# Performance work log

Measured on AMD Instinct MI355X. Metric: run time of the kernel, lower is better.

Reference implementation:

```python
import jax, jax.numpy as jnp
import numpy as np

B, D, H, E = 32768, 128, 512, 16

def setup_inputs() -> dict:
    key = jax.random.key(0)
    ks = jax.random.split(key, 5)
    x = jax.random.normal(ks[0], (B, 1, D), dtype=jnp.float32)
    s1 = 1.0 / float(np.sqrt(H))   # init_ uses last-dim size: w1 last dim = H
    s2 = 1.0 / float(np.sqrt(D))   # w2 last dim = D
    sg = 1.0 / float(np.sqrt(D))   # nn.Linear(D, E) default init scale
    w1 = jax.random.uniform(ks[1], (E, D, H), minval=-s1, maxval=s1, dtype=jnp.float32)
    w2 = jax.random.uniform(ks[2], (E, H, D), minval=-s2, maxval=s2, dtype=jnp.float32)
    wg = jax.random.uniform(ks[3], (D, E), minval=-sg, maxval=sg, dtype=jnp.float32)
    bg = jax.random.uniform(ks[4], (E,), minval=-sg, maxval=sg, dtype=jnp.float32)
    return {"x": x, "w1": w1, "w2": w2, "wg": wg, "bg": bg}

def reference(x, w1, w2, wg, bg):
    xt = x[:, 0, :]                                   # (B, D); seq dim is 1 by construction
    logits = xt @ wg + bg                             # (B, E)
    topk_vals, topk_idx = jax.lax.top_k(logits, 1)    # (B, 1) each
    scores = jax.nn.softmax(topk_vals, axis=-1)       # (B, 1); all ones for k=1
    # every expert processes every token (faithful to the reference)
    hidden = jax.nn.gelu(jnp.einsum('bd,edh->ebh', xt, w1), approximate=False)  # (E, B, H)
    eout = jnp.einsum('ebh,ehd->ebd', hidden, w2)     # (E, B, D)
    # gather selected expert per token, scale, sum over k
    sel = jnp.take_along_axis(eout.transpose(1, 0, 2), topk_idx[:, :, None], axis=1)  # (B, 1, D)
    return (sel * scores[:, :, None]).sum(axis=1)     # (B, D)
```

## Files before the change

kernel.cpp:

```cpp
#include <hip/hip_runtime.h>
#include <hip/hip_bf16.h>
#include <math.h>

#define NB 32768
#define DD 128
#define HH 512
#define EE 16
#define TM 64
#define HC 32
#define NCH (HH / HC)

typedef __attribute__((ext_vector_type(8))) short short8;
typedef __attribute__((ext_vector_type(4))) float f32x4;

__device__ __forceinline__ unsigned short f2bf(float f) {
  union { float f; unsigned u; } v; v.f = f;
  unsigned r = v.u + 0x7fffu + ((v.u >> 16) & 1u);
  return (unsigned short)(r >> 16);
}

__device__ __forceinline__ float fast_erf(float z) {
  float a = fabsf(z);
  float t = 1.0f / (1.0f + 0.3275911f * a);
  float y = t * (0.254829592f + t * (-0.284496736f + t * (1.421413741f +
            t * (-1.453152027f + t * 1.061405429f))));
  float r = 1.0f - y * __expf(-a * a);
  return z < 0.0f ? -r : r;
}

__global__ __launch_bounds__(256) void prep_kernel(
    const float* __restrict__ x, const float* __restrict__ wg,
    const float* __restrict__ bg, const float* __restrict__ w1,
    const float* __restrict__ w2, int* __restrict__ counts,
    int* __restrict__ rows, unsigned short* __restrict__ w1T,
    unsigned short* __restrict__ w2T) {
  __shared__ __align__(16) char smem[50816];
  int tid = threadIdx.x;

  if (blockIdx.x >= 512) {
    float (*tile)[65] = (float (*)[65])smem;
    int tp = blockIdx.x - 512;
    const float* src; unsigned short* dst; int S, Sd;
    if (tp < 256) {
      int e = tp >> 4, t2 = tp & 15;
      int d0 = (t2 >> 3) * 64, h0 = (t2 & 7) * 64;
      src = w1 + (size_t)e * DD * HH + (size_t)d0 * HH + h0; S = HH;
      dst = w1T + (size_t)e * HH * DD + (size_t)h0 * DD + d0; Sd = DD;
    } else {
      int t = tp - 256;
      int e = t >> 4, t2 = t & 15;
      int h0 = (t2 >> 1) * 64, d0 = (t2 & 1) * 64;
      src = w2 + (size_t)e * HH * DD + (size_t)h0 * DD + d0; S = DD;
      dst = w2T + (size_t)e * DD * HH + (size_t)d0 * HH + h0; Sd = HH;
    }
    #pragma unroll
    for (int i = 0; i < 4; ++i) {
      int u = tid + i * 256, r = u >> 4, c = (u & 15) * 4;
      float4 v = *(const float4*)(src + (size_t)r * S + c);
      tile[r][c + 0] = v.x; tile[r][c + 1] = v.y;
      tile[r][c + 2] = v.z; tile[r][c + 3] = v.w;
    }
    __syncthreads();
    #pragma unroll
    for (int i = 0; i < 4; ++i) {
      int u = tid + i * 256, tr = u >> 4, tc = (u & 15) * 4;
      ushort4 p;
      p.x = f2bf(tile[tc + 0][tr]); p.y = f2bf(tile[tc + 1][tr]);
      p.z = f2bf(tile[tc + 2][tr]); p.w = f2bf(tile[tc + 3][tr]);
      *(ushort4*)(dst + (size_t)tr * Sd + tc) = p;
    }
    return;
  }

  float  (*sx)[132] = (float (*)[132])smem;
  double (*swg)[EE] = (double (*)[EE])(smem + 33792);
  int* lcnt  = (int*)(smem + 50176);
  int* gbase = lcnt + EE;
  int* lslot = gbase + EE;
  int* lexp  = lslot + 64;

  int base = blockIdx.x * 64;
  if (tid < EE) lcnt[tid] = 0;
  for (int i = tid; i < DD * EE; i += 256) swg[i >> 4][i & 15] = (double)wg[i];
  {
    int r = tid >> 2, c0 = (tid & 3) * 32;
    const float4* src = (const float4*)(x + (size_t)(base + r) * DD + c0);
    #pragma unroll
    for (int i = 0; i < 8; ++i)
      *(float4*)&sx[r][c0 + i * 4] = src[i];
  }
  __syncthreads();

  int r = tid >> 2;
  int e0 = (tid & 3) * 4;
  double acc[4];
  #pragma unroll
  for (int j = 0; j < 4; ++j) acc[j] = (double)bg[e0 + j];

  #pragma unroll 4
  for (int d = 0; d < DD; ++d) {
    double xv = (double)sx[r][d];
    #pragma unroll
    for (int j = 0; j < 4; ++j)
      acc[j] += xv * swg[d][e0 + j];
  }

  int beste = 0; double bestv = acc[0];
  #pragma unroll
  for (int j = 1; j < 4; ++j)
    if (acc[j] > bestv) { bestv = acc[j]; beste = j; }
  int ge = e0 + beste;

  #pragma unroll
  for (int off = 1; off < 4; off <<= 1) {
    double ov = __shfl_xor(bestv, off);
    int oe = __shfl_xor(ge, off);
    if (ov > bestv || (ov == bestv && oe < ge)) { bestv = ov; ge = oe; }
  }

  if ((tid & 3) == 0) {
    lslot[r] = atomicAdd(&lcnt[ge], 1);
    lexp[r] = ge;
  }
  __syncthreads();
  if (tid < EE && lcnt[tid] > 0)
    gbase[tid] = atomicAdd(&counts[tid], lcnt[tid]);
  __syncthreads();
  if ((tid & 3) == 0) {
    int e2 = lexp[r];
    rows[e2 * NB + gbase[e2] + lslot[r]] = base + r;
  }
}

__global__ __launch_bounds__(256) void moe_gemm(
    const float* __restrict__ x, const unsigned short* __restrict__ w1T,
    const unsigned short* __restrict__ w2T, const int* __restrict__ counts,
    const int* __restrict__ rows, float* __restrict__ out) {
  int e = blockIdx.x;
  int cnt = counts[e];
  int base = blockIdx.y * TM;
  if (base >= cnt) return;

  __shared__ unsigned short sW1[2][HC][DD];
  __shared__ unsigned short sW2[2][DD][HC];
  __shared__ unsigned short sH[TM][HC];

  int tid = threadIdx.x;
  int wv = tid >> 6, l = tid & 63;
  int lm = l & 15, q = l >> 4;

  short8 xa[4];
  {
    int ridx = base + wv * 16 + lm; if (ridx >= cnt) ridx = cnt - 1;
    int grow = rows[e * NB + ridx];
    const float* xr = x + (size_t)grow * DD + q * 8;
    #pragma unroll
    for (int ks = 0; ks < 4; ++ks) {
      f32x4 v0 = *(const f32x4*)(xr + ks * 32);
      f32x4 v1 = *(const f32x4*)(xr + ks * 32 + 4);
      short8 a;
      a[0] = f2bf(v0[0]); a[1] = f2bf(v0[1]); a[2] = f2bf(v0[2]); a[3] = f2bf(v0[3]);
      a[4] = f2bf(v1[0]); a[5] = f2bf(v1[1]); a[6] = f2bf(v1[2]); a[7] = f2bf(v1[3]);
      xa[ks] = a;
    }
  }

  int r1s = tid >> 4, s1s = tid & 15;
  int sl1 = (s1s ^ (r1s & 7)) * 8;
  int r2s = tid >> 2, s2s = tid & 3;
  int sl2 = (s2s ^ ((r2s >> 1) & 3)) * 8;

  {
    const unsigned short* w1c = w1T + (size_t)e * HH * DD;
    const unsigned short* w2c = w2T + (size_t)e * DD * HH;
    uint4 a0 = *(const uint4*)(w1c + (size_t)tid * 8);
    uint4 a1 = *(const uint4*)(w1c + (size_t)(tid + 256) * 8);
    uint4 b0 = *(const uint4*)(w2c + (size_t)r2s * HH + s2s * 8);
    uint4 b1 = *(const uint4*)(w2c + (size_t)(r2s + 64) * HH + s2s * 8);
    *(uint4*)&sW1[0][r1s][sl1]      = a0;
    *(uint4*)&sW1[0][r1s + 16][sl1] = a1;
    *(uint4*)&sW2[0][r2s][sl2]      = b0;
    *(uint4*)&sW2[0][r2s + 64][sl2] = b1;
  }
  __syncthreads();

  f32x4 acc2[8];
  #pragma unroll
  for (int n = 0; n < 8; ++n) acc2[n] = (f32x4){0.f, 0.f, 0.f, 0.f};

  for (int hc = 0; hc < NCH; ++hc) {
    int b = hc & 1;

    uint4 pa0, pa1, pb0, pb1;
    if (hc + 1 < NCH) {
      const unsigned short* w1c = w1T + ((size_t)e * HH + (size_t)(hc + 1) * HC) * DD;
      const unsigned short* w2c = w2T + (size_t)e * DD * HH + (size_t)(hc + 1) * HC;
      pa0 = *(const uint4*)(w1c + (size_t)tid * 8);
      pa1 = *(const uint4*)(w1c + (size_t)(tid + 256) * 8);
      pb0 = *(const uint4*)(w2c + (size_t)r2s * HH + s2s * 8);
      pb1 = *(const uint4*)(w2c + (size_t)(r2s + 64) * HH + s2s * 8);
    }

    f32x4 acc1[2];
    #pragma unroll
    for (int n = 0; n < 2; ++n) acc1[n] = (f32x4){0.f, 0.f, 0.f, 0.f};
    #pragma unroll
    for (int ks = 0; ks < 4; ++ks) {
      #pragma unroll
      for (int n = 0; n < 2; ++n) {
        int row = n * 16 + lm;
        int sl = ((ks * 4 + q) ^ (row & 7)) * 8;
        short8 bfr = *(const short8*)&sW1[b][row][sl];
        acc1[n] = __builtin_amdgcn_mfma_f32_16x16x32_bf16(xa[ks], bfr, acc1[n], 0, 0, 0);
      }
    }
    #pragma unroll
    for (int n = 0; n < 2; ++n) {
      #pragma unroll
      for (int rr = 0; rr < 4; ++rr) {
        float v = acc1[n][rr];
        float g = 0.5f * v * (1.0f + fast_erf(v * 0.70710678118654752f));
        int row = wv * 16 + q * 4 + rr;
        int col = n * 16 + lm;
        int sl = ((col >> 3) ^ ((row >> 1) & 3)) * 8;
        sH[row][sl + (col & 7)] = f2bf(g);
      }
    }
    {
      int rowA = wv * 16 + lm;
      int slA = (q ^ ((rowA >> 1) & 3)) * 8;
      short8 a = *(const short8*)&sH[rowA][slA];
      #pragma unroll
      for (int n = 0; n < 8; ++n) {
        int row = n * 16 + lm;
        int sl = (q ^ ((row >> 1) & 3)) * 8;
        short8 bfr = *(const short8*)&sW2[b][row][sl];
        acc2[n] = __builtin_amdgcn_mfma_f32_16x16x32_bf16(a, bfr, acc2[n], 0, 0, 0);
      }
    }

    if (hc + 1 < NCH) {
      *(uint4*)&sW1[b ^ 1][r1s][sl1]      = pa0;
      *(uint4*)&sW1[b ^ 1][r1s + 16][sl1] = pa1;
      *(uint4*)&sW2[b ^ 1][r2s][sl2]      = pb0;
      *(uint4*)&sW2[b ^ 1][r2s + 64][sl2] = pb1;
    }
    __syncthreads();
  }

  #pragma unroll
  for (int rr = 0; rr < 4; ++rr) {
    int ml = wv * 16 + q * 4 + rr;
    int ridx = base + ml;
    if (ridx < cnt) {
      int grow = rows[e * NB + ridx];
      float* op = out + (size_t)grow * DD + lm;
      #pragma unroll
      for (int n = 0; n < 8; ++n) op[n * 16] = acc2[n][rr];
    }
  }
}

extern "C" void kernel_launch(void* const* d_in, const int* in_sizes, int n_in,
                              void* d_out, int out_size, void* d_ws, size_t ws_size,
                              hipStream_t stream) {
  const float* x  = (const float*)d_in[0];
  const float* w1 = (const float*)d_in[1];
  const float* w2 = (const float*)d_in[2];
  const float* wg = (const float*)d_in[3];
  const float* bg = (const float*)d_in[4];
  float* out = (float*)d_out;

  int* counts = (int*)d_ws;
  int* rows   = (int*)((char*)d_ws + 1024);
  unsigned short* w1T = (unsigned short*)((char*)d_ws + 1024 + (size_t)EE * NB * 4);
  unsigned short* w2T = w1T + (size_t)EE * HH * DD;

  hipMemsetAsync(d_ws, 0, 64, stream);
  hipLaunchKernelGGL(prep_kernel, dim3(1024), dim3(256), 0, stream,
                     x, wg, bg, w1, w2, counts, rows, w1T, w2T);
  hipLaunchKernelGGL(moe_gemm, dim3(EE, NB / TM), dim3(256), 0, stream,
                     x, w1T, w2T, counts, rows, out);
}
```

Before: 135.6 us.

## Double hidden chunk size to 64, re-swizzle LDS tiles, and use fast reciprocal in erf

Measured after the change: 170.8 us. +26.0%, slower.

```diff
diff --git a/kernel.cpp b/kernel.cpp
--- a/kernel.cpp
+++ b/kernel.cpp
@@ -7,7 +7,7 @@
 #define HH 512
 #define EE 16
 #define TM 64
-#define HC 32
+#define HC 64
 #define NCH (HH / HC)
 
 typedef __attribute__((ext_vector_type(8))) short short8;
@@ -21,7 +21,7 @@
 
 __device__ __forceinline__ float fast_erf(float z) {
   float a = fabsf(z);
-  float t = 1.0f / (1.0f + 0.3275911f * a);
+  float t = __builtin_amdgcn_rcpf(1.0f + 0.3275911f * a);
   float y = t * (0.254829592f + t * (-0.284496736f + t * (1.421413741f +
             t * (-1.453152027f + t * 1.061405429f))));
   float r = 1.0f - y * __expf(-a * a);
@@ -132,7 +132,7 @@
   }
 }
 
-__global__ __launch_bounds__(256) void moe_gemm(
+__global__ __launch_bounds__(256, 2) void moe_gemm(
     const float* __restrict__ x, const unsigned short* __restrict__ w1T,
     const unsigned short* __restrict__ w2T, const int* __restrict__ counts,
     const int* __restrict__ rows, float* __restrict__ out) {
@@ -143,7 +143,7 @@
 
   __shared__ unsigned short sW1[2][HC][DD];
   __shared__ unsigned short sW2[2][DD][HC];
-  __shared__ unsigned short sH[TM][HC];
+  __shared__ unsigned short sH[TM][72];
 
   int tid = threadIdx.x;
   int wv = tid >> 6, l = tid & 63;
@@ -168,19 +168,26 @@
   int r1s = tid >> 4, s1s = tid & 15;
   int sl1 = (s1s ^ (r1s & 7)) * 8;
   int r2s = tid >> 2, s2s = tid & 3;
-  int sl2 = (s2s ^ ((r2s >> 1) & 3)) * 8;
+  int sl2a = ((2 * s2s)     ^ (r2s & 7)) * 8;
+  int sl2b = ((2 * s2s + 1) ^ (r2s & 7)) * 8;
+
+  const unsigned short* w1e = w1T + (size_t)e * HH * DD;
+  const unsigned short* w2e = w2T + (size_t)e * DD * HH;
 
   {
-    const unsigned short* w1c = w1T + (size_t)e * HH * DD;
-    const unsigned short* w2c = w2T + (size_t)e * DD * HH;
-    uint4 a0 = *(const uint4*)(w1c + (size_t)tid * 8);
-    uint4 a1 = *(const uint4*)(w1c + (size_t)(tid + 256) * 8);
-    uint4 b0 = *(const uint4*)(w2c + (size_t)r2s * HH + s2s * 8);
-    uint4 b1 = *(const uint4*)(w2c + (size_t)(r2s + 64) * HH + s2s * 8);
-    *(uint4*)&sW1[0][r1s][sl1]      = a0;
-    *(uint4*)&sW1[0][r1s + 16][sl1] = a1;
-    *(uint4*)&sW2[0][r2s][sl2]      = b0;
-    *(uint4*)&sW2[0][r2s + 64][sl2] = b1;
+    #pragma unroll
+    for (int k = 0; k < 4; ++k) {
+      uint4 a = *(const uint4*)(w1e + (size_t)tid * 8 + (size_t)k * 2048);
+      *(uint4*)&sW1[0][r1s + 16 * k][sl1] = a;
+    }
+    uint4 b0 = *(const uint4*)(w2e + (size_t)r2s * HH + s2s * 16);
+    uint4 b1 = *(const uint4*)(w2e + (size_t)r2s * HH + s2s * 16 + 8);
+    uint4 b2 = *(const uint4*)(w2e + (size_t)(r2s + 64) * HH + s2s * 16);
+    uint4 b3 = *(const uint4*)(w2e + (size_t)(r2s + 64) * HH + s2s * 16 + 8);
+    *(uint4*)&sW2[0][r2s][sl2a]      = b0;
+    *(uint4*)&sW2[0][r2s][sl2b]      = b1;
+    *(uint4*)&sW2[0][r2s + 64][sl2a] = b2;
+    *(uint4*)&sW2[0][r2s + 64][sl2b] = b3;
   }
   __syncthreads();
 
@@ -191,23 +198,26 @@
   for (int hc = 0; hc < NCH; ++hc) {
     int b = hc & 1;
 
-    uint4 pa0, pa1, pb0, pb1;
+    uint4 pa[4], pb[4];
     if (hc + 1 < NCH) {
-      const unsigned short* w1c = w1T + ((size_t)e * HH + (size_t)(hc + 1) * HC) * DD;
-      const unsigned short* w2c = w2T + (size_t)e * DD * HH + (size_t)(hc + 1) * HC;
-      pa0 = *(const uint4*)(w1c + (size_t)tid * 8);
-      pa1 = *(const uint4*)(w1c + (size_t)(tid + 256) * 8);
-      pb0 = *(const uint4*)(w2c + (size_t)r2s * HH + s2s * 8);
-      pb1 = *(const uint4*)(w2c + (size_t)(r2s + 64) * HH + s2s * 8);
-    }
-
-    f32x4 acc1[2];
-    #pragma unroll
-    for (int n = 0; n < 2; ++n) acc1[n] = (f32x4){0.f, 0.f, 0.f, 0.f};
+      const unsigned short* w1c = w1e + (size_t)(hc + 1) * HC * DD;
+      const unsigned short* w2c = w2e + (size_t)(hc + 1) * HC;
+      #pragma unroll
+      for (int k = 0; k < 4; ++k)
+        pa[k] = *(const uint4*)(w1c + (size_t)tid * 8 + (size_t)k * 2048);
+      pb[0] = *(const uint4*)(w2c + (size_t)r2s * HH + s2s * 16);
+      pb[1] = *(const uint4*)(w2c + (size_t)r2s * HH + s2s * 16 + 8);
+      pb[2] = *(const uint4*)(w2c + (size_t)(r2s + 64) * HH + s2s * 16);
+      pb[3] = *(const uint4*)(w2c + (size_t)(r2s + 64) * HH + s2s * 16 + 8);
+    }
+
+    f32x4 acc1[4];
+    #pragma unroll
+    for (int n = 0; n < 4; ++n) acc1[n] = (f32x4){0.f, 0.f, 0.f, 0.f};
     #pragma unroll
     for (int ks = 0; ks < 4; ++ks) {
       #pragma unroll
-      for (int n = 0; n < 2; ++n) {
+      for (int n = 0; n < 4; ++n) {
         int row = n * 16 + lm;
         int sl = ((ks * 4 + q) ^ (row & 7)) * 8;
         short8 bfr = *(const short8*)&sW1[b][row][sl];
@@ -215,35 +225,35 @@
       }
     }
     #pragma unroll
-    for (int n = 0; n < 2; ++n) {
+    for (int n = 0; n < 4; ++n) {
       #pragma unroll
       for (int rr = 0; rr < 4; ++rr) {
         float v = acc1[n][rr];
         float g = 0.5f * v * (1.0f + fast_erf(v * 0.70710678118654752f));
-        int row = wv * 16 + q * 4 + rr;
-        int col = n * 16 + lm;
-        int sl = ((col >> 3) ^ ((row >> 1) & 3)) * 8;
-        sH[row][sl + (col & 7)] = f2bf(g);
+        sH[wv * 16 + q * 4 + rr][n * 16 + lm] = f2bf(g);
       }
     }
-    {
-      int rowA = wv * 16 + lm;
-      int slA = (q ^ ((rowA >> 1) & 3)) * 8;
-      short8 a = *(const short8*)&sH[rowA][slA];
+    #pragma unroll
+    for (int ks = 0; ks < 2; ++ks) {
+      int kk = ks * 32 + q * 8;
+      short8 a = *(const short8*)&sH[wv * 16 + lm][kk];
       #pragma unroll
       for (int n = 0; n < 8; ++n) {
         int row = n * 16 + lm;
-        int sl = (q ^ ((row >> 1) & 3)) * 8;
+        int sl = ((ks * 4 + q) ^ (row & 7)) * 8;
         short8 bfr = *(const short8*)&sW2[b][row][sl];
         acc2[n] = __builtin_amdgcn_mfma_f32_16x16x32_bf16(a, bfr, acc2[n], 0, 0, 0);
       }
     }
 
     if (hc + 1 < NCH) {
-      *(uint4*)&sW1[b ^ 1][r1s][sl1]      = pa0;
-      *(uint4*)&sW1[b ^ 1][r1s + 16][sl1] = pa1;
-      *(uint4*)&sW2[b ^ 1][r2s][sl2]      = pb0;
-      *(uint4*)&sW2[b ^ 1][r2s + 64][sl2] = pb1;
+      #pragma unroll
+      for (int k = 0; k < 4; ++k)
+        *(uint4*)&sW1[b ^ 1][r1s + 16 * k][sl1] = pa[k];
+      *(uint4*)&sW2[b ^ 1][r2s][sl2a]      = pb[0];
+      *(uint4*)&sW2[b ^ 1][r2s][sl2b]      = pb[1];
+      *(uint4*)&sW2[b ^ 1][r2s + 64][sl2a] = pb[2];
+      *(uint4*)&sW2[b ^ 1][r2s + 64][sl2b] = pb[3];
     }
     __syncthreads();
   }
```
